# Kernel optimization log

Measured on AMD Instinct MI355X. Metric: run time of the kernel, lower is better.

Reference implementation:

```python
import jax, jax.numpy as jnp
import numpy as np

B, T, C = 16, 2048, 512
G = 2                 # groups
V = 320               # num_vars
D = C // G            # var_dim = 256
GAMMA = 0.25
GN_EPS = 1e-5


def setup_inputs() -> dict:
    key = jax.random.key(0)
    k1, k2, k3 = jax.random.split(key, 3)
    x = jax.random.normal(k1, (B, T, C), dtype=jnp.float32)
    # grouped 1x1 conv weight: (out_channels, in_channels_per_group) = (C, D)
    conv_w = jax.random.normal(k2, (C, D), dtype=jnp.float32) * (1.0 / np.sqrt(D))
    gn_w = jnp.ones((C,), dtype=jnp.float32)
    gn_b = jnp.zeros((C,), dtype=jnp.float32)
    embedding = 0.01 * jax.random.normal(k3, (V, G, D), dtype=jnp.float32)
    return {"x": x, "conv_w": conv_w, "gn_w": gn_w, "gn_b": gn_b, "embedding": embedding}


def reference(x, conv_w, gn_w, gn_b, embedding):
    # x: [B, T, C] (time_first=True) -> [B, C, T]
    xt = jnp.transpose(x, (0, 2, 1))
    # grouped 1x1 conv == per-group matmul
    xg = xt.reshape(B, G, D, T)                      # [B, G, D_in, T]
    wg = conv_w.reshape(G, D, D)                     # [G, D_out, D_in]
    h = jnp.einsum('bgit,goi->bgot', xg, wg)         # [B, G, D, T]
    # Fp32GroupNorm over (D, T) per (B, G)
    mu = h.mean(axis=(2, 3), keepdims=True)
    var = ((h - mu) ** 2).mean(axis=(2, 3), keepdims=True)
    hn = (h - mu) * jax.lax.rsqrt(var + GN_EPS)
    ze = hn.reshape(B, C, T) * gn_w[None, :, None] + gn_b[None, :, None]  # [B, C, T]

    ze_ = ze.reshape(B, G, D, T).transpose(0, 3, 1, 2)  # [B, T, G, D]
    # squared distances to codebook (same argmin as L2 norm)
    e_sq = (embedding ** 2).sum(-1).T                    # [G, V]
    d2 = ((ze_ ** 2).sum(-1)[..., None]
          - 2.0 * jnp.einsum('btgd,vgd->btgv', ze_, embedding)
          + e_sq[None, None])                            # [B, T, G, V]
    idx = jnp.argmin(d2, axis=-1)                        # [B, T, G] int32

    zq = embedding[idx, jnp.arange(G)[None, None, :]]    # [B, T, G, D]
    zq = zq.reshape(B, T, C).transpose(0, 2, 1)          # [B, C, T]

    # straight-through
    x_st = jax.lax.stop_gradient(zq) + (ze - jax.lax.stop_gradient(ze))
    x_out = jnp.transpose(x_st, (0, 2, 1))               # back to [B, T, C]

    # code perplexity from one-hot usage counts
    flat_idx = idx.reshape(-1, G)                        # [B*T, G]
    counts = jnp.zeros((V, G), dtype=jnp.float32).at[flat_idx, jnp.arange(G)[None, :]].add(1.0)
    hard_probs = counts.T / jnp.float32(B * T)           # [G, V]
    code_perplexity = jnp.exp(-jnp.sum(hard_probs * jnp.log(hard_probs + 1e-7), axis=-1)).sum()

    latent_loss = jnp.mean((zq - jax.lax.stop_gradient(ze)) ** 2)
    commitment_loss = jnp.mean((ze - jax.lax.stop_gradient(zq)) ** 2)
    kmeans_loss = latent_loss + GAMMA * commitment_loss
    return x_out, kmeans_loss, code_perplexity
```

## Files before the change

kernel.cpp:

```cpp
#include <hip/hip_runtime.h>
#include <math.h>

#define BB 16
#define TT 2048
#define CC 512
#define GG 2
#define DD 256
#define VV 320
#define DT (DD*TT)
#define NOUT ((size_t)BB*TT*CC)

#define OFF_H      0ULL
#define SZ_H       ((size_t)BB*GG*TT*DD*4)
#define OFF_PART   (OFF_H + SZ_H)
#define OFF_MUSIG  (OFF_PART + 4096ULL*2*8)
#define OFF_ESQ    (OFF_MUSIG + 32ULL*2*4)
#define OFF_CNT    (OFF_ESQ + (size_t)GG*VV*4)
#define OFF_LOSS   (OFF_CNT + (size_t)GG*VV*4)
#define OFF_EMBH   67180032ULL
#define OFF_WH     (OFF_EMBH + 327680ULL)
#define OFF_WL     (OFF_WH + 262144ULL)

typedef _Float16 half8   __attribute__((ext_vector_type(8)));
typedef float    f32x4   __attribute__((ext_vector_type(4)));

#define MARGIN 2e-3f
#define CAP 16

#define GLOAD_LDS16(g, l) \
  __builtin_amdgcn_global_load_lds((const __attribute__((address_space(1))) void*)(g), \
                                   (__attribute__((address_space(3))) void*)(l), 16, 0, 0)

__global__ __launch_bounds__(256) void k_emb(const float* __restrict__ emb,
                                             const float* __restrict__ w,
                                             _Float16* __restrict__ embHp,
                                             _Float16* __restrict__ wHp,
                                             _Float16* __restrict__ wLp,
                                             float* __restrict__ esq,
                                             unsigned* __restrict__ counts,
                                             float* __restrict__ loss) {
  int blk = blockIdx.x;
  int tid = threadIdx.x;
  if (blk == 40) {
    for (int i = tid; i < GG*VV; i += 256) counts[i] = 0u;
    if (tid == 0) *loss = 0.0f;
    return;
  }
  if (blk >= 41) {
    int wblk = blk - 41;
    int g = wblk >> 3, c = wblk & 7;
    int o = tid;
    const float* wrow = w + (size_t)(g*DD + o)*DD + (c << 5);
    #pragma unroll
    for (int hgrp = 0; hgrp < 4; ++hgrp) {
      float4 f1 = *(const float4*)(wrow + (hgrp << 2));
      float4 f2 = *(const float4*)(wrow + (hgrp << 2) + 16);
      float fv[8] = {f1.x, f1.y, f1.z, f1.w, f2.x, f2.y, f2.z, f2.w};
      half8 vh, vl;
      #pragma unroll
      for (int e = 0; e < 8; ++e) {
        _Float16 hh = (_Float16)fv[e];
        vh[e] = hh;
        vl[e] = (_Float16)(fv[e] - (float)hh);
      }
      size_t base = (((((size_t)(g*8 + c)) << 2) + hgrp) << 8) + o;
      *(half8*)(wHp + (base << 3)) = vh;
      *(half8*)(wLp + (base << 3)) = vl;
    }
    return;
  }
  int g = blk / 20;
  int v0 = (blk % 20) * 16;
  int vl = tid >> 4, dl = tid & 15;
  int v = v0 + vl;
  double sq = 0.0;
  #pragma unroll
  for (int k = 0; k < 16; k++) {
    int d = dl + (k << 4);
    float e = emb[((size_t)v*GG + g)*DD + d];
    sq += (double)e * (double)e;
  }
  #pragma unroll
  for (int m = 1; m < 16; m <<= 1) sq += __shfl_xor(sq, m);
  if (dl == 0) esq[g*VV + v] = (float)sq;

  const int hgrp = dl >> 2, jb = dl & 3;
  #pragma unroll
  for (int c = 0; c < 8; ++c) {
    int k0 = (c << 5) + (hgrp << 2) + jb;
    int k1 = k0 + 16;
    float e0 = emb[((size_t)v*GG + g)*DD + k0];
    float e1 = emb[((size_t)v*GG + g)*DD + k1];
    size_t base = (((size_t)(g*8 + c)*4 + hgrp)*320 + v)*8;
    embHp[base + jb]     = (_Float16)e0;
    embHp[base + jb + 4] = (_Float16)e1;
  }
}

__global__ __launch_bounds__(256, 2) void k_conv2(const float* __restrict__ x,
                                                  const _Float16* __restrict__ wH,
                                                  const _Float16* __restrict__ wL,
                                                  float* __restrict__ h,
                                                  double* __restrict__ part) {
  __shared__ __align__(16) char BsC[65536];
  __shared__ double r1[4], r2[4];
  const int bid = blockIdx.x;
  const int bg = bid >> 4, tt = bid & 15;
  const int b = bg >> 1, g = bg & 1;
  const int tid = threadIdx.x;
  const int wv = tid >> 6, lane = tid & 63;
  const int l15 = tid & 15, lh = lane >> 4;
  const int t0w = (tt << 7) + (wv << 5);

  f32x4 acc[2][16];
  #pragma unroll
  for (int tf = 0; tf < 2; ++tf)
    #pragma unroll
    for (int vf = 0; vf < 16; ++vf) acc[tf][vf] = 0.0f;

  const char* WHg = (const char*)(wH + ((size_t)g << 16));
  const char* WLg = (const char*)(wL + ((size_t)g << 16));
  const float* xb0 = x + ((size_t)(b*TT + t0w + l15)*CC + g*DD + (lh << 2));
  const float* xb1 = xb0 + ((size_t)16)*CC;

  {
    const char* sH = WHg + wv*4096 + lane*16;
    const char* sL = WLg + wv*4096 + lane*16;
    char* dH = BsC + wv*4096;
    char* dL = BsC + 32768 + wv*4096;
    #pragma unroll
    for (int i = 0; i < 4; ++i) {
      GLOAD_LDS16(sH + i*1024, dH + i*1024);
      GLOAD_LDS16(sL + i*1024, dL + i*1024);
    }
  }
  float4 p00 = *(const float4*)(xb0);
  float4 p01 = *(const float4*)(xb0 + 16);
  float4 p10 = *(const float4*)(xb1);
  float4 p11 = *(const float4*)(xb1 + 16);

  int cur = 0;
  #pragma unroll 1
  for (int c = 0; c < 8; ++c) {
    if (c < 7) {
      const char* sH = WHg + (size_t)(c + 1)*16384 + wv*4096 + lane*16;
      const char* sL = WLg + (size_t)(c + 1)*16384 + wv*4096 + lane*16;
      char* dH = BsC + (cur ^ 1)*16384 + wv*4096;
      char* dL = BsC + 32768 + (cur ^ 1)*16384 + wv*4096;
      #pragma unroll
      for (int i = 0; i < 4; ++i) {
        GLOAD_LDS16(sH + i*1024, dH + i*1024);
        GLOAD_LDS16(sL + i*1024, dL + i*1024);
      }
      asm volatile("s_waitcnt vmcnt(12)" ::: "memory");
    } else {
      asm volatile("s_waitcnt vmcnt(4)" ::: "memory");
    }
    __builtin_amdgcn_s_barrier();

    float4 c00 = p00, c01 = p01, c10 = p10, c11 = p11;
    if (c < 7) {
      const int off = (c + 1) << 5;
      p00 = *(const float4*)(xb0 + off);
      p01 = *(const float4*)(xb0 + off + 16);
      p10 = *(const float4*)(xb1 + off);
      p11 = *(const float4*)(xb1 + off + 16);
    }
    half8 ah[2], al[2];
    {
      float fv0[8] = {c00.x, c00.y, c00.z, c00.w, c01.x, c01.y, c01.z, c01.w};
      float fv1[8] = {c10.x, c10.y, c10.z, c10.w, c11.x, c11.y, c11.z, c11.w};
      #pragma unroll
      for (int e = 0; e < 8; ++e) {
        _Float16 h0 = (_Float16)fv0[e];
        ah[0][e] = h0; al[0][e] = (_Float16)(fv0[e] - (float)h0);
        _Float16 h1 = (_Float16)fv1[e];
        ah[1][e] = h1; al[1][e] = (_Float16)(fv1[e] - (float)h1);
      }
    }
    const char* BH = BsC + cur*16384;
    const char* BL = BsC + 32768 + cur*16384;
    #pragma unroll
    for (int vf = 0; vf < 16; ++vf) {
      const int o = (vf << 4) + l15;
      const int bo = ((lh << 8) + o) << 4;
      half8 bh = *(const half8*)(BH + bo);
      half8 bl = *(const half8*)(BL + bo);
      #pragma unroll
      for (int tf = 0; tf < 2; ++tf) {
        acc[tf][vf] = __builtin_amdgcn_mfma_f32_16x16x32_f16(ah[tf], bh, acc[tf][vf], 0, 0, 0);
        acc[tf][vf] = __builtin_amdgcn_mfma_f32_16x16x32_f16(al[tf], bh, acc[tf][vf], 0, 0, 0);
        acc[tf][vf] = __builtin_amdgcn_mfma_f32_16x16x32_f16(ah[tf], bl, acc[tf][vf], 0, 0, 0);
      }
    }
    __builtin_amdgcn_s_barrier();
    cur ^= 1;
  }

  double s1 = 0.0, s2 = 0.0;
  {
    float* hb = h + (size_t)bg*TT*DD;
    #pragma unroll
    for (int tf = 0; tf < 2; ++tf) {
      #pragma unroll
      for (int reg = 0; reg < 4; ++reg) {
        const int t = t0w + (tf << 4) + (lh << 2) + reg;
        float* hrow = hb + (size_t)t*DD + l15;
        #pragma unroll
        for (int vf = 0; vf < 16; ++vf) {
          float v = acc[tf][vf][reg];
          hrow[vf << 4] = v;
          double dv = (double)v;
          s1 += dv; s2 += dv*dv;
        }
      }
    }
  }
  #pragma unroll
  for (int m = 32; m > 0; m >>= 1) { s1 += __shfl_down(s1, m); s2 += __shfl_down(s2, m); }
  if (lane == 0) { r1[wv] = s1; r2[wv] = s2; }
  __syncthreads();
  if (tid == 0) {
    part[(size_t)bid*2]     = r1[0] + r1[1] + r1[2] + r1[3];
    part[(size_t)bid*2 + 1] = r2[0] + r2[1] + r2[2] + r2[3];
  }
}

__global__ __launch_bounds__(256, 3) void k_vq2(const float* __restrict__ h,
                                                const double* __restrict__ part,
                                                const float* __restrict__ gn_w,
                                                const float* __restrict__ gn_b,
                                                const _Float16* __restrict__ embH,
                                                const float* __restrict__ esq,
                                                const float* __restrict__ emb,
                                                float* __restrict__ out,
                                                unsigned* __restrict__ counts,
                                                float* __restrict__ loss) {
  __shared__ __align__(16) char smem[43008];
  float*  esqs    = (float*)smem;
  int*    candcnt = (int*)(smem + 1280);
  int*    bestv   = (int*)(smem + 1536);
  int*    slowl   = (int*)(smem + 1792);
  int*    nslow   = (int*)(smem + 2048);
  float*  ze2s    = (float*)(smem + 2112);
  float*  ymins   = (float*)(smem + 2368);
  float*  lossrow = (float*)(smem + 2624);
  unsigned short* cand = (unsigned short*)(smem + 2880);
  float*  gnws    = (float*)(smem + 40960);
  float*  gnbs    = (float*)(smem + 41984);

  const int bid = blockIdx.x;
  const int bg  = bid >> 5;
  const int t0  = (bid & 31) << 6;
  const int b = bg >> 1, g = bg & 1;
  const int tid = threadIdx.x;
  const int lane = tid & 63, wv = tid >> 6;
  const int l15 = tid & 15, lh = lane >> 4;

  float mu, rs;
  {
    double s1 = 0.0, s2 = 0.0;
    const double* pp = part + (size_t)bg*32;
    for (int r = 0; r < 16; r++) { s1 += pp[r*2]; s2 += pp[r*2 + 1]; }
    double mud = s1 / (double)DT;
    double var = s2 / (double)DT - mud*mud;
    double rsd = 1.0 / sqrt(var + 1e-5);
    mu = (float)mud;
    rs = (float)rsd;
  }

  const float* hb = h + ((size_t)bg*TT + t0)*DD;
  const char* gBH = (const char*)(embH + (size_t)(g*8)*10240);
  const float* gwp = gn_w + g*DD;
  const float* gbp = gn_b + g*DD;

  gnws[tid] = gwp[tid];
  gnbs[tid] = gbp[tid];
  __syncthreads();

  f32x4 acc[20];
  #pragma unroll
  for (int vf = 0; vf < 20; ++vf) acc[vf] = 0.0f;

  const float* hb0 = hb + (size_t)((wv << 4) + l15)*DD + (lh << 2);

  float4 a00 = *(const float4*)(hb0);
  float4 a01 = *(const float4*)(hb0 + 16);
  float4 n00 = *(const float4*)(hb0 + 32);
  float4 n01 = *(const float4*)(hb0 + 48);
  asm volatile("" ::: "memory");
  {
    const char* sB = gBH + wv*5120 + lane*16;
    char* dB = smem + wv*5120;
    #pragma unroll
    for (int i = 0; i < 5; ++i) GLOAD_LDS16(sB + i*1024, dB + i*1024);
  }

  float ze2acc = 0.0f;
  #pragma unroll
  for (int c = 0; c < 8; ++c) {
    const int cu = c & 1;
    if (c < 7) {
      const char* sB = gBH + (size_t)(c + 1)*20480 + wv*5120 + lane*16;
      char* dB = smem + (cu ^ 1)*20480 + wv*5120;
      #pragma unroll
      for (int i = 0; i < 5; ++i) GLOAD_LDS16(sB + i*1024, dB + i*1024);
    }
    asm volatile("" ::: "memory");
    float4 f00 = a00, f01 = a01;
    if (c < 6) {
      const int off = (c + 2) << 5;
      f00 = *(const float4*)(hb0 + off);
      f01 = *(const float4*)(hb0 + off + 16);
    }
    if (c == 7)                 { asm volatile("s_waitcnt vmcnt(0)" ::: "memory"); }
    else if (c == 0 || c == 6)  { asm volatile("s_waitcnt vmcnt(7)" ::: "memory"); }
    else                        { asm volatile("s_waitcnt vmcnt(9)" ::: "memory"); }
    __builtin_amdgcn_s_barrier();

    const int c32 = c << 5;
    half8 ah;
    {
      float4 w1 = *(const float4*)(gnws + c32 + (lh << 2));
      float4 w2 = *(const float4*)(gnws + c32 + (lh << 2) + 16);
      float4 b1 = *(const float4*)(gnbs + c32 + (lh << 2));
      float4 b2 = *(const float4*)(gnbs + c32 + (lh << 2) + 16);
      float fv[8]  = {a00.x, a00.y, a00.z, a00.w, a01.x, a01.y, a01.z, a01.w};
      float wv_[8] = {w1.x, w1.y, w1.z, w1.w, w2.x, w2.y, w2.z, w2.w};
      float bv_[8] = {b1.x, b1.y, b1.z, b1.w, b2.x, b2.y, b2.z, b2.w};
      #pragma unroll
      for (int e = 0; e < 8; ++e) {
        float z = __fmul_rn(__fsub_rn(fv[e], mu), rs);
        z = __fadd_rn(__fmul_rn(z, wv_[e]), bv_[e]);
        ah[e] = (_Float16)z;
        ze2acc = fmaf(z, z, ze2acc);
      }
    }
    const char* BH = smem + cu*20480;
    #pragma unroll
    for (int vf = 0; vf < 20; ++vf) {
      const int v = (vf << 4) + l15;
      half8 bh = *(const half8*)(BH + ((lh*320 + v) << 4));
      acc[vf] = __builtin_amdgcn_mfma_f32_16x16x32_f16(ah, bh, acc[vf], 0, 0, 0);
    }
    __builtin_amdgcn_s_barrier();
    a00 = n00; a01 = n01; n00 = f00; n01 = f01;
  }
  __syncthreads();

  if (tid < 160) { esqs[tid] = esq[g*VV + tid]; esqs[tid + 160] = esq[g*VV + tid + 160]; }
  if (tid < 64) { candcnt[tid] = 0; bestv[tid] = -1; }
  if (tid == 0) *nslow = 0;
  {
    float s = ze2acc;
    s += __shfl_down(s, 32);
    s += __shfl_down(s, 16);
    if (lane < 16) ze2s[(wv << 4) + l15] = s;
  }
  __syncthreads();

  #pragma unroll
  for (int reg = 0; reg < 4; ++reg) {
    int row = (wv << 4) + (lh << 2) + reg;
    float y[20]; float mn = 3.4e38f;
    #pragma unroll
    for (int vf = 0; vf < 20; ++vf) {
      y[vf] = fmaf(-2.0f, acc[vf][reg], esqs[(vf << 4) + l15]);
      mn = fminf(mn, y[vf]);
    }
    #pragma unroll
    for (int m = 1; m < 16; m <<= 1) mn = fminf(mn, __shfl_xor(mn, m));
    if (l15 == 0) ymins[row] = mn;
    float thr = mn + MARGIN;
    #pragma unroll
    for (int vf = 0; vf < 20; ++vf) {
      if (y[vf] <= thr) {
        int pos = atomicAdd(&candcnt[row], 1);
        if (pos < CAP) cand[row*CAP + pos] = (unsigned short)((vf << 4) + l15);
      }
    }
  }
  __syncthreads();
  if (tid < 64) {
    int cnt = candcnt[tid];
    if (cnt == 1) {
      bestv[tid] = cand[tid*CAP];
      lossrow[tid] = ze2s[tid] + ymins[tid];
    } else {
      int p = atomicAdd(nslow, 1); slowl[p] = tid;
    }
  }
  __syncthreads();

  const int ns = *nslow;
  for (int i = wv; i < ns; i += 4) {
    const int row = slowl[i];
    float4 hx  = *(const float4*)(hb + (size_t)row*DD + (lane << 2));
    float4 gw4 = *(const float4*)(gwp + (lane << 2));
    float4 gb4 = *(const float4*)(gbp + (lane << 2));
    float hv[4] = {hx.x, hx.y, hx.z, hx.w};
    float gwv[4] = {gw4.x, gw4.y, gw4.z, gw4.w};
    float gbv[4] = {gb4.x, gb4.y, gb4.z, gb4.w};
    float zf[4];
    #pragma unroll
    for (int e = 0; e < 4; ++e) {
      float z = __fmul_rn(__fsub_rn(hv[e], mu), rs);
      zf[e] = __fadd_rn(__fmul_rn(z, gwv[e]), gbv[e]);
    }
    int cnt = candcnt[row];
    double bd = 1e300; int bvv = 0x7fffffff;
    if (cnt <= CAP) {
      for (int ci = 0; ci < cnt; ++ci) {
        int v = cand[row*CAP + ci];
        float4 ev = *(const float4*)(emb + ((size_t)v*GG + g)*DD + (lane << 2));
        float evv[4] = {ev.x, ev.y, ev.z, ev.w};
        double s = 0.0;
        #pragma unroll
        for (int e = 0; e < 4; ++e) {
          double df = (double)zf[e] - (double)evv[e];
          s += df*df;
        }
        #pragma unroll
        for (int m = 32; m > 0; m >>= 1) s += __shfl_down(s, m);
        s = __shfl(s, 0);
        if (s < bd || (s == bd && v < bvv)) { bd = s; bvv = v; }
      }
    } else {
      for (int v = 0; v < VV; ++v) {
        float4 ev = *(const float4*)(emb + ((size_t)v*GG + g)*DD + (lane << 2));
        float evv[4] = {ev.x, ev.y, ev.z, ev.w};
        double s = 0.0;
        #pragma unroll
        for (int e = 0; e < 4; ++e) {
          double df = (double)zf[e] - (double)evv[e];
          s += df*df;
        }
        #pragma unroll
        for (int m = 32; m > 0; m >>= 1) s += __shfl_down(s, m);
        s = __shfl(s, 0);
        if (s < bd) { bd = s; bvv = v; }
      }
    }
    if (lane == 0) { bestv[row] = bvv; lossrow[row] = (float)bd; }
  }
  __syncthreads();

  if (tid < 64) atomicAdd(&counts[g*VV + bestv[tid]], 1u);
  if (wv == 0) {
    float s = lossrow[lane];
    #pragma unroll
    for (int m = 32; m > 0; m >>= 1) s += __shfl_down(s, m);
    if (lane == 0) atomicAdd(loss, s);
  }

  float* ob = out + (size_t)(b*TT + t0)*CC + g*DD + tid;
  #pragma unroll 1
  for (int r0 = 0; r0 < 64; r0 += 8) {
    int vv[8]; float ee[8];
    #pragma unroll
    for (int j = 0; j < 8; ++j) vv[j] = bestv[r0 + j];
    #pragma unroll
    for (int j = 0; j < 8; ++j) ee[j] = emb[((size_t)vv[j]*GG + g)*DD + tid];
    #pragma unroll
    for (int j = 0; j < 8; ++j) ob[(size_t)(r0 + j)*CC] = ee[j];
  }
}

__global__ __launch_bounds__(256) void k_final(const unsigned* __restrict__ counts,
                                               const float* __restrict__ loss,
                                               float* __restrict__ out) {
  __shared__ float sd[256];
  int tid = threadIdx.x;
  float perp = 0.0f;
  for (int g = 0; g < GG; g++) {
    float p1 = 0.0f;
    for (int v = tid; v < VV; v += 256) {
      float p = (float)counts[g*VV + v] / 32768.0f;
      p1 += p * logf(p + 1e-7f);
    }
    sd[tid] = p1;
    __syncthreads();
    for (int s = 128; s > 0; s >>= 1) {
      if (tid < s) sd[tid] += sd[tid + s];
      __syncthreads();
    }
    if (tid == 0) perp += expf(-sd[0]);
    __syncthreads();
  }
  if (tid == 0) {
    out[NOUT]     = 1.25f * (*loss) / (float)NOUT;
    out[NOUT + 1] = perp;
  }
}

extern "C" void kernel_launch(void* const* d_in, const int* in_sizes, int n_in,
                              void* d_out, int out_size, void* d_ws, size_t ws_size,
                              hipStream_t stream) {
  const float* x   = (const float*)d_in[0];
  const float* cw  = (const float*)d_in[1];
  const float* gnw = (const float*)d_in[2];
  const float* gnb = (const float*)d_in[3];
  const float* emb = (const float*)d_in[4];
  float* out = (float*)d_out;
  char* ws = (char*)d_ws;
  float*     h      = (float*)(ws + OFF_H);
  double*    part   = (double*)(ws + OFF_PART);
  float*     esq    = (float*)(ws + OFF_ESQ);
  unsigned*  counts = (unsigned*)(ws + OFF_CNT);
  float*     loss   = (float*)(ws + OFF_LOSS);
  _Float16*  embH   = (_Float16*)(ws + OFF_EMBH);
  _Float16*  wH     = (_Float16*)(ws + OFF_WH);
  _Float16*  wL     = (_Float16*)(ws + OFF_WL);

  hipLaunchKernelGGL(k_emb,   dim3(57),   dim3(256), 0, stream,
                     emb, cw, embH, wH, wL, esq, counts, loss);
  hipLaunchKernelGGL(k_conv2, dim3(512),  dim3(256), 0, stream, x, wH, wL, h, part);
  hipLaunchKernelGGL(k_vq2,   dim3(1024), dim3(256), 0, stream,
                     h, part, gnw, gnb, embH, esq, emb, out, counts, loss);
  hipLaunchKernelGGL(k_final, dim3(1),    dim3(256), 0, stream, counts, loss, out);
}
```

Measured before the change: 99.66 us.

## Double rows per VQ block to reuse staged codebook across two MFMA tiles

k_vq2 now handles 128 time rows per block instead of 64, so each wave computes two 16-row MFMA tiles that share each codebook fragment read from LDS. The grid is halved to 512 blocks, which halves the total codebook traffic from global memory to LDS. The activation prefetch changes from two chunks ahead to one chunk ahead, and the waitcnt values are updated to match. The cost is doubled accumulator registers (occupancy hint lowered from 3 to 2 blocks per CU) and fewer blocks in flight to hide latency.

New measurement: 98.13 us. No clear change (-1.5%).

```diff
diff --git a/kernel.cpp b/kernel.cpp
--- a/kernel.cpp
+++ b/kernel.cpp
@@ -226,7 +226,7 @@
   }
 }
 
-__global__ __launch_bounds__(256, 3) void k_vq2(const float* __restrict__ h,
+__global__ __launch_bounds__(256, 2) void k_vq2(const float* __restrict__ h,
                                                 const double* __restrict__ part,
                                                 const float* __restrict__ gn_w,
                                                 const float* __restrict__ gn_b,
@@ -239,19 +239,19 @@
   __shared__ __align__(16) char smem[43008];
   float*  esqs    = (float*)smem;
   int*    candcnt = (int*)(smem + 1280);
-  int*    bestv   = (int*)(smem + 1536);
-  int*    slowl   = (int*)(smem + 1792);
-  int*    nslow   = (int*)(smem + 2048);
-  float*  ze2s    = (float*)(smem + 2112);
-  float*  ymins   = (float*)(smem + 2368);
-  float*  lossrow = (float*)(smem + 2624);
-  unsigned short* cand = (unsigned short*)(smem + 2880);
+  int*    bestv   = (int*)(smem + 1792);
+  int*    slowl   = (int*)(smem + 2304);
+  int*    nslow   = (int*)(smem + 2816);
+  float*  ze2s    = (float*)(smem + 2880);
+  float*  ymins   = (float*)(smem + 3392);
+  float*  lossrow = (float*)(smem + 3904);
+  unsigned short* cand = (unsigned short*)(smem + 4416);
   float*  gnws    = (float*)(smem + 40960);
   float*  gnbs    = (float*)(smem + 41984);
 
   const int bid = blockIdx.x;
-  const int bg  = bid >> 5;
-  const int t0  = (bid & 31) << 6;
+  const int bg  = bid >> 4;
+  const int t0  = (bid & 15) << 7;
   const int b = bg >> 1, g = bg & 1;
   const int tid = threadIdx.x;
   const int lane = tid & 63, wv = tid >> 6;
@@ -278,25 +278,28 @@
   gnbs[tid] = gbp[tid];
   __syncthreads();
 
-  f32x4 acc[20];
-  #pragma unroll
-  for (int vf = 0; vf < 20; ++vf) acc[vf] = 0.0f;
-
-  const float* hb0 = hb + (size_t)((wv << 4) + l15)*DD + (lh << 2);
-
-  float4 a00 = *(const float4*)(hb0);
-  float4 a01 = *(const float4*)(hb0 + 16);
-  float4 n00 = *(const float4*)(hb0 + 32);
-  float4 n01 = *(const float4*)(hb0 + 48);
-  asm volatile("" ::: "memory");
+  f32x4 acc[2][20];
+  #pragma unroll
+  for (int tf = 0; tf < 2; ++tf)
+    #pragma unroll
+    for (int vf = 0; vf < 20; ++vf) acc[tf][vf] = 0.0f;
+
+  const float* hr0 = hb + (size_t)((wv << 5) + l15)*DD + (lh << 2);
+  const float* hr1 = hr0 + ((size_t)16)*DD;
+
   {
     const char* sB = gBH + wv*5120 + lane*16;
     char* dB = smem + wv*5120;
     #pragma unroll
     for (int i = 0; i < 5; ++i) GLOAD_LDS16(sB + i*1024, dB + i*1024);
   }
-
-  float ze2acc = 0.0f;
+  asm volatile("" ::: "memory");
+  float4 a00 = *(const float4*)(hr0);
+  float4 a01 = *(const float4*)(hr0 + 16);
+  float4 a10 = *(const float4*)(hr1);
+  float4 a11 = *(const float4*)(hr1 + 16);
+
+  float ze2a0 = 0.0f, ze2a1 = 0.0f;
   #pragma unroll
   for (int c = 0; c < 8; ++c) {
     const int cu = c & 1;
@@ -307,33 +310,39 @@
       for (int i = 0; i < 5; ++i) GLOAD_LDS16(sB + i*1024, dB + i*1024);
     }
     asm volatile("" ::: "memory");
-    float4 f00 = a00, f01 = a01;
-    if (c < 6) {
-      const int off = (c + 2) << 5;
-      f00 = *(const float4*)(hb0 + off);
-      f01 = *(const float4*)(hb0 + off + 16);
-    }
-    if (c == 7)                 { asm volatile("s_waitcnt vmcnt(0)" ::: "memory"); }
-    else if (c == 0 || c == 6)  { asm volatile("s_waitcnt vmcnt(7)" ::: "memory"); }
-    else                        { asm volatile("s_waitcnt vmcnt(9)" ::: "memory"); }
+    float4 n00, n01, n10, n11;
+    if (c < 7) {
+      const int off = (c + 1) << 5;
+      n00 = *(const float4*)(hr0 + off);
+      n01 = *(const float4*)(hr0 + off + 16);
+      n10 = *(const float4*)(hr1 + off);
+      n11 = *(const float4*)(hr1 + off + 16);
+    }
+    if (c < 7) { asm volatile("s_waitcnt vmcnt(13)" ::: "memory"); }
+    else       { asm volatile("s_waitcnt vmcnt(4)"  ::: "memory"); }
     __builtin_amdgcn_s_barrier();
 
     const int c32 = c << 5;
-    half8 ah;
+    half8 ah[2];
     {
       float4 w1 = *(const float4*)(gnws + c32 + (lh << 2));
       float4 w2 = *(const float4*)(gnws + c32 + (lh << 2) + 16);
       float4 b1 = *(const float4*)(gnbs + c32 + (lh << 2));
       float4 b2 = *(const float4*)(gnbs + c32 + (lh << 2) + 16);
-      float fv[8]  = {a00.x, a00.y, a00.z, a00.w, a01.x, a01.y, a01.z, a01.w};
       float wv_[8] = {w1.x, w1.y, w1.z, w1.w, w2.x, w2.y, w2.z, w2.w};
       float bv_[8] = {b1.x, b1.y, b1.z, b1.w, b2.x, b2.y, b2.z, b2.w};
+      float f0[8] = {a00.x, a00.y, a00.z, a00.w, a01.x, a01.y, a01.z, a01.w};
+      float f1[8] = {a10.x, a10.y, a10.z, a10.w, a11.x, a11.y, a11.z, a11.w};
       #pragma unroll
       for (int e = 0; e < 8; ++e) {
-        float z = __fmul_rn(__fsub_rn(fv[e], mu), rs);
-        z = __fadd_rn(__fmul_rn(z, wv_[e]), bv_[e]);
-        ah[e] = (_Float16)z;
-        ze2acc = fmaf(z, z, ze2acc);
+        float z0 = __fmul_rn(__fsub_rn(f0[e], mu), rs);
+        z0 = __fadd_rn(__fmul_rn(z0, wv_[e]), bv_[e]);
+        ah[0][e] = (_Float16)z0;
+        ze2a0 = fmaf(z0, z0, ze2a0);
+        float z1 = __fmul_rn(__fsub_rn(f1[e], mu), rs);
+        z1 = __fadd_rn(__fmul_rn(z1, wv_[e]), bv_[e]);
+        ah[1][e] = (_Float16)z1;
+        ze2a1 = fmaf(z1, z1, ze2a1);
       }
     }
     const char* BH = smem + cu*20480;
@@ -341,47 +350,55 @@
     for (int vf = 0; vf < 20; ++vf) {
       const int v = (vf << 4) + l15;
       half8 bh = *(const half8*)(BH + ((lh*320 + v) << 4));
-      acc[vf] = __builtin_amdgcn_mfma_f32_16x16x32_f16(ah, bh, acc[vf], 0, 0, 0);
+      acc[0][vf] = __builtin_amdgcn_mfma_f32_16x16x32_f16(ah[0], bh, acc[0][vf], 0, 0, 0);
+      acc[1][vf] = __builtin_amdgcn_mfma_f32_16x16x32_f16(ah[1], bh, acc[1][vf], 0, 0, 0);
     }
     __builtin_amdgcn_s_barrier();
-    a00 = n00; a01 = n01; n00 = f00; n01 = f01;
+    if (c < 7) { a00 = n00; a01 = n01; a10 = n10; a11 = n11; }
   }
   __syncthreads();
 
   if (tid < 160) { esqs[tid] = esq[g*VV + tid]; esqs[tid + 160] = esq[g*VV + tid + 160]; }
-  if (tid < 64) { candcnt[tid] = 0; bestv[tid] = -1; }
+  if (tid < 128) { candcnt[tid] = 0; bestv[tid] = -1; }
   if (tid == 0) *nslow = 0;
   {
-    float s = ze2acc;
+    float s = ze2a0;
     s += __shfl_down(s, 32);
     s += __shfl_down(s, 16);
-    if (lane < 16) ze2s[(wv << 4) + l15] = s;
-  }
-  __syncthreads();
-
-  #pragma unroll
-  for (int reg = 0; reg < 4; ++reg) {
-    int row = (wv << 4) + (lh << 2) + reg;
-    float y[20]; float mn = 3.4e38f;
-    #pragma unroll
-    for (int vf = 0; vf < 20; ++vf) {
-      y[vf] = fmaf(-2.0f, acc[vf][reg], esqs[(vf << 4) + l15]);
-      mn = fminf(mn, y[vf]);
-    }
-    #pragma unroll
-    for (int m = 1; m < 16; m <<= 1) mn = fminf(mn, __shfl_xor(mn, m));
-    if (l15 == 0) ymins[row] = mn;
-    float thr = mn + MARGIN;
-    #pragma unroll
-    for (int vf = 0; vf < 20; ++vf) {
-      if (y[vf] <= thr) {
-        int pos = atomicAdd(&candcnt[row], 1);
-        if (pos < CAP) cand[row*CAP + pos] = (unsigned short)((vf << 4) + l15);
-      }
-    }
-  }
-  __syncthreads();
-  if (tid < 64) {
+    if (lane < 16) ze2s[(wv << 5) + l15] = s;
+    float t = ze2a1;
+    t += __shfl_down(t, 32);
+    t += __shfl_down(t, 16);
+    if (lane < 16) ze2s[(wv << 5) + 16 + l15] = t;
+  }
+  __syncthreads();
+
+  #pragma unroll
+  for (int tf = 0; tf < 2; ++tf) {
+    #pragma unroll
+    for (int reg = 0; reg < 4; ++reg) {
+      int row = (wv << 5) + (tf << 4) + (lh << 2) + reg;
+      float y[20]; float mn = 3.4e38f;
+      #pragma unroll
+      for (int vf = 0; vf < 20; ++vf) {
+        y[vf] = fmaf(-2.0f, acc[tf][vf][reg], esqs[(vf << 4) + l15]);
+        mn = fminf(mn, y[vf]);
+      }
+      #pragma unroll
+      for (int m = 1; m < 16; m <<= 1) mn = fminf(mn, __shfl_xor(mn, m));
+      if (l15 == 0) ymins[row] = mn;
+      float thr = mn + MARGIN;
+      #pragma unroll
+      for (int vf = 0; vf < 20; ++vf) {
+        if (y[vf] <= thr) {
+          int pos = atomicAdd(&candcnt[row], 1);
+          if (pos < CAP) cand[row*CAP + pos] = (unsigned short)((vf << 4) + l15);
+        }
+      }
+    }
+  }
+  __syncthreads();
+  if (tid < 128) {
     int cnt = candcnt[tid];
     if (cnt == 1) {
       bestv[tid] = cand[tid*CAP];
@@ -445,9 +462,9 @@
   }
   __syncthreads();
 
-  if (tid < 64) atomicAdd(&counts[g*VV + bestv[tid]], 1u);
+  if (tid < 128) atomicAdd(&counts[g*VV + bestv[tid]], 1u);
   if (wv == 0) {
-    float s = lossrow[lane];
+    float s = lossrow[lane] + lossrow[lane + 64];
     #pragma unroll
     for (int m = 32; m > 0; m >>= 1) s += __shfl_down(s, m);
     if (lane == 0) atomicAdd(loss, s);
@@ -455,7 +472,7 @@
 
   float* ob = out + (size_t)(b*TT + t0)*CC + g*DD + tid;
   #pragma unroll 1
-  for (int r0 = 0; r0 < 64; r0 += 8) {
+  for (int r0 = 0; r0 < 128; r0 += 8) {
     int vv[8]; float ee[8];
     #pragma unroll
     for (int j = 0; j < 8; ++j) vv[j] = bestv[r0 + j];
@@ -515,7 +532,7 @@
   hipLaunchKernelGGL(k_emb,   dim3(57),   dim3(256), 0, stream,
                      emb, cw, embH, wH, wL, esq, counts, loss);
   hipLaunchKernelGGL(k_conv2, dim3(512),  dim3(256), 0, stream, x, wH, wL, h, part);
-  hipLaunchKernelGGL(k_vq2,   dim3(1024), dim3(256), 0, stream,
+  hipLaunchKernelGGL(k_vq2,   dim3(512),  dim3(256), 0, stream,
                      h, part, gnw, gnb, embH, esq, emb, out, counts, loss);
   hipLaunchKernelGGL(k_final, dim3(1),    dim3(256), 0, stream, counts, loss, out);
 }
```

## Double VQ block to 128 rows with 512 threads, staging codebook in two halves

Applied to the files above, without the earlier changes.

The VQ scoring kernel now uses 512-thread blocks covering 128 time rows instead of 64. The fp16 codebook is loaded into 80KB of LDS in two halves, so each codebook load is shared by twice as many rows, replacing the finer double-buffered pipeline. The output gather now writes float4 per lane per row. This trades away the overlap of loads with MFMA work and register prefetch of h, and the larger LDS footprint limits how many blocks fit per CU.

Result: no change. 99.34 us (-0.3%).

```diff
diff --git a/kernel.cpp b/kernel.cpp
--- a/kernel.cpp
+++ b/kernel.cpp
@@ -226,32 +226,32 @@
   }
 }
 
-__global__ __launch_bounds__(256, 3) void k_vq2(const float* __restrict__ h,
-                                                const double* __restrict__ part,
-                                                const float* __restrict__ gn_w,
-                                                const float* __restrict__ gn_b,
-                                                const _Float16* __restrict__ embH,
-                                                const float* __restrict__ esq,
-                                                const float* __restrict__ emb,
-                                                float* __restrict__ out,
-                                                unsigned* __restrict__ counts,
-                                                float* __restrict__ loss) {
-  __shared__ __align__(16) char smem[43008];
+__global__ __launch_bounds__(512, 2) void k_score(const float* __restrict__ h,
+                                                  const double* __restrict__ part,
+                                                  const float* __restrict__ gn_w,
+                                                  const float* __restrict__ gn_b,
+                                                  const _Float16* __restrict__ embH,
+                                                  const float* __restrict__ esq,
+                                                  const float* __restrict__ emb,
+                                                  float* __restrict__ out,
+                                                  unsigned* __restrict__ counts,
+                                                  float* __restrict__ loss) {
+  __shared__ __align__(16) char smem[83968];
   float*  esqs    = (float*)smem;
   int*    candcnt = (int*)(smem + 1280);
-  int*    bestv   = (int*)(smem + 1536);
-  int*    slowl   = (int*)(smem + 1792);
-  int*    nslow   = (int*)(smem + 2048);
-  float*  ze2s    = (float*)(smem + 2112);
-  float*  ymins   = (float*)(smem + 2368);
-  float*  lossrow = (float*)(smem + 2624);
-  unsigned short* cand = (unsigned short*)(smem + 2880);
-  float*  gnws    = (float*)(smem + 40960);
-  float*  gnbs    = (float*)(smem + 41984);
+  int*    bestv   = (int*)(smem + 1792);
+  int*    slowl   = (int*)(smem + 2304);
+  int*    nslow   = (int*)(smem + 2816);
+  float*  ze2s    = (float*)(smem + 2880);
+  float*  ymins   = (float*)(smem + 3392);
+  float*  lossrow = (float*)(smem + 3904);
+  unsigned short* cand = (unsigned short*)(smem + 4416);
+  float*  gnws    = (float*)(smem + 81920);
+  float*  gnbs    = (float*)(smem + 82944);
 
   const int bid = blockIdx.x;
-  const int bg  = bid >> 5;
-  const int t0  = (bid & 31) << 6;
+  const int bg  = bid >> 4;
+  const int t0  = (bid & 15) << 7;
   const int b = bg >> 1, g = bg & 1;
   const int tid = threadIdx.x;
   const int lane = tid & 63, wv = tid >> 6;
@@ -274,82 +274,64 @@
   const float* gwp = gn_w + g*DD;
   const float* gbp = gn_b + g*DD;
 
-  gnws[tid] = gwp[tid];
-  gnbs[tid] = gbp[tid];
+  if (tid < 256) { gnws[tid] = gwp[tid]; gnbs[tid] = gbp[tid]; }
   __syncthreads();
 
   f32x4 acc[20];
   #pragma unroll
   for (int vf = 0; vf < 20; ++vf) acc[vf] = 0.0f;
 
-  const float* hb0 = hb + (size_t)((wv << 4) + l15)*DD + (lh << 2);
-
-  float4 a00 = *(const float4*)(hb0);
-  float4 a01 = *(const float4*)(hb0 + 16);
-  float4 n00 = *(const float4*)(hb0 + 32);
-  float4 n01 = *(const float4*)(hb0 + 48);
-  asm volatile("" ::: "memory");
-  {
-    const char* sB = gBH + wv*5120 + lane*16;
-    char* dB = smem + wv*5120;
-    #pragma unroll
-    for (int i = 0; i < 5; ++i) GLOAD_LDS16(sB + i*1024, dB + i*1024);
-  }
+  const float* hr0 = hb + (size_t)((wv << 4) + l15)*DD + (lh << 2);
 
   float ze2acc = 0.0f;
-  #pragma unroll
-  for (int c = 0; c < 8; ++c) {
-    const int cu = c & 1;
-    if (c < 7) {
-      const char* sB = gBH + (size_t)(c + 1)*20480 + wv*5120 + lane*16;
-      char* dB = smem + (cu ^ 1)*20480 + wv*5120;
-      #pragma unroll
-      for (int i = 0; i < 5; ++i) GLOAD_LDS16(sB + i*1024, dB + i*1024);
-    }
-    asm volatile("" ::: "memory");
-    float4 f00 = a00, f01 = a01;
-    if (c < 6) {
-      const int off = (c + 2) << 5;
-      f00 = *(const float4*)(hb0 + off);
-      f01 = *(const float4*)(hb0 + off + 16);
-    }
-    if (c == 7)                 { asm volatile("s_waitcnt vmcnt(0)" ::: "memory"); }
-    else if (c == 0 || c == 6)  { asm volatile("s_waitcnt vmcnt(7)" ::: "memory"); }
-    else                        { asm volatile("s_waitcnt vmcnt(9)" ::: "memory"); }
-    __builtin_amdgcn_s_barrier();
-
-    const int c32 = c << 5;
-    half8 ah;
+  #pragma unroll 1
+  for (int C = 0; C < 2; ++C) {
     {
+      const char* sB = gBH + (size_t)C*81920 + wv*10240 + lane*16;
+      char* dB = smem + wv*10240;
+      #pragma unroll
+      for (int i = 0; i < 10; ++i) GLOAD_LDS16(sB + i*1024, dB + i*1024);
+    }
+    asm volatile("s_waitcnt vmcnt(0)" ::: "memory");
+    __syncthreads();
+
+    #pragma unroll
+    for (int sc = 0; sc < 4; ++sc) {
+      const int c = (C << 2) + sc;
+      const int c32 = c << 5;
+      float4 f1 = *(const float4*)(hr0 + c32);
+      float4 f2 = *(const float4*)(hr0 + c32 + 16);
       float4 w1 = *(const float4*)(gnws + c32 + (lh << 2));
       float4 w2 = *(const float4*)(gnws + c32 + (lh << 2) + 16);
       float4 b1 = *(const float4*)(gnbs + c32 + (lh << 2));
       float4 b2 = *(const float4*)(gnbs + c32 + (lh << 2) + 16);
-      float fv[8]  = {a00.x, a00.y, a00.z, a00.w, a01.x, a01.y, a01.z, a01.w};
-      float wv_[8] = {w1.x, w1.y, w1.z, w1.w, w2.x, w2.y, w2.z, w2.w};
-      float bv_[8] = {b1.x, b1.y, b1.z, b1.w, b2.x, b2.y, b2.z, b2.w};
-      #pragma unroll
-      for (int e = 0; e < 8; ++e) {
-        float z = __fmul_rn(__fsub_rn(fv[e], mu), rs);
-        z = __fadd_rn(__fmul_rn(z, wv_[e]), bv_[e]);
-        ah[e] = (_Float16)z;
-        ze2acc = fmaf(z, z, ze2acc);
-      }
-    }
-    const char* BH = smem + cu*20480;
-    #pragma unroll
-    for (int vf = 0; vf < 20; ++vf) {
-      const int v = (vf << 4) + l15;
-      half8 bh = *(const half8*)(BH + ((lh*320 + v) << 4));
-      acc[vf] = __builtin_amdgcn_mfma_f32_16x16x32_f16(ah, bh, acc[vf], 0, 0, 0);
-    }
-    __builtin_amdgcn_s_barrier();
-    a00 = n00; a01 = n01; n00 = f00; n01 = f01;
+      half8 ah;
+      {
+        float fv[8]  = {f1.x, f1.y, f1.z, f1.w, f2.x, f2.y, f2.z, f2.w};
+        float wv_[8] = {w1.x, w1.y, w1.z, w1.w, w2.x, w2.y, w2.z, w2.w};
+        float bv_[8] = {b1.x, b1.y, b1.z, b1.w, b2.x, b2.y, b2.z, b2.w};
+        #pragma unroll
+        for (int e = 0; e < 8; ++e) {
+          float z = __fmul_rn(__fsub_rn(fv[e], mu), rs);
+          z = __fadd_rn(__fmul_rn(z, wv_[e]), bv_[e]);
+          ah[e] = (_Float16)z;
+          ze2acc = fmaf(z, z, ze2acc);
+        }
+      }
+      const char* BH = smem + sc*20480;
+      #pragma unroll
+      for (int vf = 0; vf < 20; ++vf) {
+        const int v = (vf << 4) + l15;
+        half8 bh = *(const half8*)(BH + ((lh*320 + v) << 4));
+        acc[vf] = __builtin_amdgcn_mfma_f32_16x16x32_f16(ah, bh, acc[vf], 0, 0, 0);
+      }
+    }
+    if (C == 0) __syncthreads();
   }
   __syncthreads();
 
   if (tid < 160) { esqs[tid] = esq[g*VV + tid]; esqs[tid + 160] = esq[g*VV + tid + 160]; }
-  if (tid < 64) { candcnt[tid] = 0; bestv[tid] = -1; }
+  if (tid < 128) { candcnt[tid] = 0; bestv[tid] = -1; }
   if (tid == 0) *nslow = 0;
   {
     float s = ze2acc;
@@ -381,7 +363,7 @@
     }
   }
   __syncthreads();
-  if (tid < 64) {
+  if (tid < 128) {
     int cnt = candcnt[tid];
     if (cnt == 1) {
       bestv[tid] = cand[tid*CAP];
@@ -393,7 +375,7 @@
   __syncthreads();
 
   const int ns = *nslow;
-  for (int i = wv; i < ns; i += 4) {
+  for (int i = wv; i < ns; i += 8) {
     const int row = slowl[i];
     float4 hx  = *(const float4*)(hb + (size_t)row*DD + (lane << 2));
     float4 gw4 = *(const float4*)(gwp + (lane << 2));
@@ -445,24 +427,28 @@
   }
   __syncthreads();
 
-  if (tid < 64) atomicAdd(&counts[g*VV + bestv[tid]], 1u);
+  if (tid < 128) atomicAdd(&counts[g*VV + bestv[tid]], 1u);
   if (wv == 0) {
-    float s = lossrow[lane];
+    float s = lossrow[lane] + lossrow[lane + 64];
     #pragma unroll
     for (int m = 32; m > 0; m >>= 1) s += __shfl_down(s, m);
     if (lane == 0) atomicAdd(loss, s);
   }
 
-  float* ob = out + (size_t)(b*TT + t0)*CC + g*DD + tid;
   #pragma unroll 1
-  for (int r0 = 0; r0 < 64; r0 += 8) {
-    int vv[8]; float ee[8];
-    #pragma unroll
-    for (int j = 0; j < 8; ++j) vv[j] = bestv[r0 + j];
-    #pragma unroll
-    for (int j = 0; j < 8; ++j) ee[j] = emb[((size_t)vv[j]*GG + g)*DD + tid];
-    #pragma unroll
-    for (int j = 0; j < 8; ++j) ob[(size_t)(r0 + j)*CC] = ee[j];
+  for (int r0 = 0; r0 < 16; r0 += 4) {
+    int vv[4]; float4 ee[4];
+    #pragma unroll
+    for (int j = 0; j < 4; ++j) vv[j] = bestv[(wv << 4) + r0 + j];
+    #pragma unroll
+    for (int j = 0; j < 4; ++j)
+      ee[j] = *(const float4*)(emb + ((size_t)vv[j]*GG + g)*DD + (lane << 2));
+    #pragma unroll
+    for (int j = 0; j < 4; ++j) {
+      const int row = (wv << 4) + r0 + j;
+      float* op = out + ((size_t)(b*TT + t0 + row))*CC + g*DD + (lane << 2);
+      *(float4*)op = ee[j];
+    }
   }
 }
 
@@ -515,7 +501,7 @@
   hipLaunchKernelGGL(k_emb,   dim3(57),   dim3(256), 0, stream,
                      emb, cw, embH, wH, wL, esq, counts, loss);
   hipLaunchKernelGGL(k_conv2, dim3(512),  dim3(256), 0, stream, x, wH, wL, h, part);
-  hipLaunchKernelGGL(k_vq2,   dim3(1024), dim3(256), 0, stream,
+  hipLaunchKernelGGL(k_score, dim3(512),  dim3(512), 0, stream,
                      h, part, gnw, gnb, embH, esq, emb, out, counts, loss);
   hipLaunchKernelGGL(k_final, dim3(1),    dim3(256), 0, stream, counts, loss, out);
 }
```
